# Kernel tuning notes

Measured on AMD Instinct MI355X. Metric: run time of the kernel, lower is better.

The kernel has to match this reference:

```python
import jax, jax.numpy as jnp
import numpy as np

B, N, C_IN = 2, 2048, 256
H, C_H = 8, 32  # no_heads, c_hidden; H*C_H == 256


def setup_inputs() -> dict:
    key = jax.random.key(0)
    ks = jax.random.split(key, 10)
    s_in = 1.0 / np.sqrt(C_IN)
    s_hid = 1.0 / np.sqrt(H * C_H)
    return {
        "q_x": jax.random.normal(ks[0], (B, N, C_IN), dtype=jnp.float32),
        "kv_x": jax.random.normal(ks[1], (B, N, C_IN), dtype=jnp.float32),
        "bias": jax.random.normal(ks[2], (B, H, N, N), dtype=jnp.float32),
        # Linear weights stored as [in, out] (transpose of torch layout)
        "Wq": jax.random.normal(ks[3], (C_IN, H * C_H), dtype=jnp.float32) * s_in,
        "Wk": jax.random.normal(ks[4], (C_IN, H * C_H), dtype=jnp.float32) * s_in,
        "Wv": jax.random.normal(ks[5], (C_IN, H * C_H), dtype=jnp.float32) * s_in,
        "Wg": jax.random.normal(ks[6], (C_IN, H * C_H), dtype=jnp.float32) * s_in,
        "bg": jnp.zeros((H * C_H,), dtype=jnp.float32),
        "Wo": jax.random.normal(ks[7], (H * C_H, C_IN), dtype=jnp.float32) * s_hid,
        "bo": jnp.zeros((C_IN,), dtype=jnp.float32),
    }


def reference(q_x, kv_x, bias, Wq, Wk, Wv, Wg, bg, Wo, bo):
    inv_sqrt = 1.0 / jnp.sqrt(jnp.asarray(C_H, q_x.dtype))
    # projections -> [B, N, H, C_H]
    q = (q_x @ Wq).reshape(B, N, H, C_H) * inv_sqrt
    k = (kv_x @ Wk).reshape(B, N, H, C_H)
    v = (kv_x @ Wv).reshape(B, N, H, C_H)
    # attention scores [B, H, Nq, Nk] with added pairwise bias
    a = jnp.einsum("bqhc,bkhc->bhqk", q, k) + bias
    a = jax.nn.softmax(a, axis=-1)
    o = jnp.einsum("bhqk,bkhc->bqhc", a, v)  # [B, N, H, C_H]
    # sigmoid gating
    g = jax.nn.sigmoid(q_x @ Wg + bg).reshape(B, N, H, C_H)
    o = o * g
    # output projection
    return o.reshape(B, N, H * C_H) @ Wo + bo
```

## Files before the change

kernel.cpp:

```cpp
#include <hip/hip_runtime.h>
#include <hip/hip_bf16.h>

#define B_   2
#define N_   2048
#define CIN  256
#define NH   8
#define CH   32

typedef unsigned short u16;
typedef __attribute__((ext_vector_type(4))) float f32x4;
typedef __bf16 bf16x8 __attribute__((ext_vector_type(8)));
typedef u16 u16x4 __attribute__((ext_vector_type(4)));
typedef u16 u16x8 __attribute__((ext_vector_type(8)));

static __device__ __forceinline__ u16 b16(float f) {
    __bf16 h = (__bf16)f;
    union { __bf16 h; u16 u; } c; c.h = h; return c.u;
}
static __device__ __forceinline__ float bf2f(u16 u) {
    union { unsigned u; float f; } c; c.u = ((unsigned)u) << 16; return c.f;
}
static __device__ __forceinline__ float sigmoidf_(float x) {
    return 1.0f / (1.0f + __expf(-x));
}
static __device__ __forceinline__ void gload_lds16(const void* g, void* lds) {
    __builtin_amdgcn_global_load_lds(
        (const __attribute__((address_space(1))) unsigned int*)g,
        (__attribute__((address_space(3))) unsigned int*)lds, 16, 0, 0);
}

__global__ __launch_bounds__(256)
void prep_kernel(const float* __restrict__ qx, const float* __restrict__ kvx,
                 u16* __restrict__ qxb, u16* __restrict__ kvxb,
                 const float* __restrict__ Wq, const float* __restrict__ Wk,
                 const float* __restrict__ Wv, const float* __restrict__ Wg,
                 const float* __restrict__ Wo,
                 u16* __restrict__ WqT, u16* __restrict__ WkT,
                 u16* __restrict__ WvT, u16* __restrict__ WgT,
                 u16* __restrict__ WoT)
{
    const int flat = blockIdx.x;
    const int tid = threadIdx.x;
    if (flat < 1024) {
        const int t = flat * 256 + tid;
        const int which = t >> 17;
        const size_t i = (size_t)(t & 131071) * 8;
        const float* s = which ? kvx : qx;
        u16* d = which ? kvxb : qxb;
        float4 a = *(const float4*)&s[i];
        float4 bv = *(const float4*)&s[i + 4];
        u16x8 o;
        o[0] = b16(a.x);  o[1] = b16(a.y);  o[2] = b16(a.z);  o[3] = b16(a.w);
        o[4] = b16(bv.x); o[5] = b16(bv.y); o[6] = b16(bv.z); o[7] = b16(bv.w);
        *(u16x8*)&d[i] = o;
        return;
    }
    const int wz = flat - 1024;
    const int z = wz >> 4, t16 = wz & 15;
    const int k0 = (t16 & 3) * 64, n0 = (t16 >> 2) * 64;
    const float* W = (z == 0) ? Wq : (z == 1) ? Wk : (z == 2) ? Wv : (z == 3) ? Wg : Wo;
    u16* Wt = (z == 0) ? WqT : (z == 1) ? WkT : (z == 2) ? WvT : (z == 3) ? WgT : WoT;
    const float s = (z == 0) ? 0.17677669529663687f : 1.0f;

    __shared__ float T[64][65];
    const int a = tid >> 4, c4 = (tid & 15) * 4;
#pragma unroll
    for (int i = 0; i < 4; i++) {
        float4 v = *(const float4*)&W[(size_t)(k0 + a + i * 16) * CIN + n0 + c4];
        T[a + i * 16][c4 + 0] = v.x * s; T[a + i * 16][c4 + 1] = v.y * s;
        T[a + i * 16][c4 + 2] = v.z * s; T[a + i * 16][c4 + 3] = v.w * s;
    }
    __syncthreads();
#pragma unroll
    for (int i = 0; i < 4; i++) {
        const int nr = a + i * 16;
        u16x4 o;
        o[0] = b16(T[c4 + 0][nr]); o[1] = b16(T[c4 + 1][nr]);
        o[2] = b16(T[c4 + 2][nr]); o[3] = b16(T[c4 + 3][nr]);
        *(u16x4*)&Wt[(size_t)(n0 + nr) * CIN + k0 + c4] = o;
    }
}

__global__ __launch_bounds__(256)
void proj_mfma(const u16* __restrict__ qxb, const u16* __restrict__ kvxb,
               const u16* __restrict__ WqT, const u16* __restrict__ WkT,
               const u16* __restrict__ WvT, const u16* __restrict__ WgT,
               const float* __restrict__ bgv,
               u16* __restrict__ Qw, u16* __restrict__ Kw,
               u16* __restrict__ Vt, u16* __restrict__ Gw)
{
    const int z = blockIdx.z;
    const int tid = threadIdx.x, w = tid >> 6, l = tid & 63, lr = l & 15, lq = l >> 4;
    f32x4 acc[4] = {{0,0,0,0},{0,0,0,0},{0,0,0,0},{0,0,0,0}};

    if (z != 2) {
        const u16* A = (z == 1) ? kvxb : qxb;
        const u16* W = (z == 0) ? WqT : (z == 1) ? WkT : WgT;
        const int m0 = blockIdx.y * 64 + w * 16;
        const int n0 = blockIdx.x * 64;
        const u16* Ap = A + (size_t)(m0 + lr) * CIN + lq * 8;
        const u16* Wp = W + (size_t)(n0 + lr) * CIN + lq * 8;
#pragma unroll
        for (int k0 = 0; k0 < CIN; k0 += 32) {
            bf16x8 af = *(const bf16x8*)(Ap + k0);
#pragma unroll
            for (int nt = 0; nt < 4; nt++) {
                bf16x8 bf = *(const bf16x8*)(Wp + (size_t)nt * 16 * CIN + k0);
                acc[nt] = __builtin_amdgcn_mfma_f32_16x16x32_bf16(af, bf, acc[nt], 0, 0, 0);
            }
        }
        if (z == 3) {
#pragma unroll
            for (int nt = 0; nt < 4; nt++) {
                const int col = n0 + nt * 16 + lr;
                const float bb = bgv[col];
#pragma unroll
                for (int r = 0; r < 4; r++)
                    Gw[(size_t)(m0 + lq * 4 + r) * CIN + col] = b16(sigmoidf_(acc[nt][r] + bb));
            }
        } else {
            u16* D = (z == 0) ? Qw : Kw;
#pragma unroll
            for (int nt = 0; nt < 4; nt++)
#pragma unroll
                for (int r = 0; r < 4; r++)
                    D[(size_t)(m0 + lq * 4 + r) * CIN + n0 + nt * 16 + lr] = b16(acc[nt][r]);
        }
    } else {
        const int c0 = blockIdx.x * 64 + w * 16;
        const int n0g = blockIdx.y * 64;
        const int bb_ = n0g >> 11, nl0 = n0g & (N_ - 1);
        const u16* Ap = WvT + (size_t)(c0 + lr) * CIN + lq * 8;
        const u16* Bp = kvxb + (size_t)(n0g + lr) * CIN + lq * 8;
#pragma unroll
        for (int k0 = 0; k0 < CIN; k0 += 32) {
            bf16x8 af = *(const bf16x8*)(Ap + k0);
#pragma unroll
            for (int nt = 0; nt < 4; nt++) {
                bf16x8 bf = *(const bf16x8*)(Bp + (size_t)nt * 16 * CIN + k0);
                acc[nt] = __builtin_amdgcn_mfma_f32_16x16x32_bf16(af, bf, acc[nt], 0, 0, 0);
            }
        }
#pragma unroll
        for (int nt = 0; nt < 4; nt++)
#pragma unroll
            for (int r = 0; r < 4; r++)
                Vt[((size_t)bb_ * CIN + c0 + lq * 4 + r) * N_ + nl0 + nt * 16 + lr] = b16(acc[nt][r]);
    }
}

#define RMAX(x) { x = fmaxf(x, __shfl_xor(x, 1)); x = fmaxf(x, __shfl_xor(x, 2)); \
                  x = fmaxf(x, __shfl_xor(x, 4)); x = fmaxf(x, __shfl_xor(x, 8)); }
#define RSUM(x) { x += __shfl_xor(x, 1); x += __shfl_xor(x, 2); \
                  x += __shfl_xor(x, 4); x += __shfl_xor(x, 8); }

__global__ __launch_bounds__(256)
void attn_kernel(const u16* __restrict__ Qw, const u16* __restrict__ Kw,
                 const u16* __restrict__ Vt, const float* __restrict__ bias,
                 const u16* __restrict__ Gw, u16* __restrict__ Owg)
{
    const int bid = blockIdx.x;
    const int h = bid & 7, qt = (bid >> 3) & 31, b = bid >> 8;
    const int tid = threadIdx.x;
    const int w = tid >> 6, l = tid & 63, lr = l & 15, lq = l >> 4;
    const int qb = qt * 64;

    __shared__ __align__(16) float Bt[4][3][16][32];
    __shared__ u16 Plds[4][8][4][16];

    const bf16x8 qf = *(const bf16x8*)(Qw + (size_t)(b * N_ + qb + w * 16 + lr) * CIN + h * CH + lq * 8);
    const u16* Kb = Kw + (size_t)(b * N_ + lr) * CIN + h * CH + lq * 8;
    const u16* Vb = Vt + (size_t)((b * NH + h) * CH + lr) * N_ + lq * 8;
    const float* biasW = bias + ((size_t)(b * NH + h) * N_ + qb + w * 16) * N_;

    const float* gl0 = biasW + (size_t)(l >> 3) * N_ + (l & 7) * 4;
    const float* gl1 = biasW + (size_t)(8 + (l >> 3)) * N_ + (l & 7) * 4;

#define STAGE(TT, BI) { \
    gload_lds16(gl0 + (size_t)(TT) * 32, &Bt[w][BI][0][0]); \
    gload_lds16(gl1 + (size_t)(TT) * 32, &Bt[w][BI][8][0]); }

#define KVLOAD(K) { kf0 = *(const bf16x8*)(Kb + (size_t)(K) * CIN); \
                    kf1 = *(const bf16x8*)(Kb + (size_t)((K) + 16) * CIN); \
                    vf0 = *(const bf16x8*)(Vb + (K)); \
                    vf1 = *(const bf16x8*)(Vb + 16 * N_ + (K)); }

    f32x4 acc0 = {0.f, 0.f, 0.f, 0.f}, acc1 = {0.f, 0.f, 0.f, 0.f};
    float m0v = 8.f, m1v = 8.f, m2v = 8.f, m3v = 8.f;
    float l0 = 0.f, l1 = 0.f, l2 = 0.f, l3 = 0.f;
    bf16x8 kf0, kf1, vf0, vf1;

    STAGE(0, 0)
    __builtin_amdgcn_sched_barrier(0);
    KVLOAD(0)
    __builtin_amdgcn_sched_barrier(0);
    STAGE(1, 1)
    __builtin_amdgcn_sched_barrier(0);

    int cur = 0, nxt = 2;
    for (int t = 0; t < 64; t++) {
        asm volatile("s_waitcnt vmcnt(2)" ::: "memory");
        const bf16x8 ck0 = kf0, ck1 = kf1, cv0 = vf0, cv1 = vf1;
        KVLOAD(((t + 1) & 63) * 32)
        __builtin_amdgcn_sched_barrier(0);
        STAGE((t + 2) & 63, nxt)
        __builtin_amdgcn_sched_barrier(0);

        const float* bt = &Bt[w][cur][lq * 4][0];
        f32x4 c0, c1;
        c0[0] = bt[0 * 32 + lr];      c0[1] = bt[1 * 32 + lr];
        c0[2] = bt[2 * 32 + lr];      c0[3] = bt[3 * 32 + lr];
        c1[0] = bt[0 * 32 + 16 + lr]; c1[1] = bt[1 * 32 + 16 + lr];
        c1[2] = bt[2 * 32 + 16 + lr]; c1[3] = bt[3 * 32 + 16 + lr];

        f32x4 s0 = __builtin_amdgcn_mfma_f32_16x16x32_bf16(qf, ck0, c0, 0, 0, 0);
        f32x4 s1 = __builtin_amdgcn_mfma_f32_16x16x32_bf16(qf, ck1, c1, 0, 0, 0);

        float pm0 = fmaxf(s0[0], s1[0]);
        float pm1 = fmaxf(s0[1], s1[1]);
        float pm2 = fmaxf(s0[2], s1[2]);
        float pm3 = fmaxf(s0[3], s1[3]);
        bool ev = (pm0 > m0v) || (pm1 > m1v) || (pm2 > m2v) || (pm3 > m3v);
        if (__any(ev)) {
            RMAX(pm0) RMAX(pm1) RMAX(pm2) RMAX(pm3)
            float t0 = fmaxf(m0v, pm0), t1 = fmaxf(m1v, pm1);
            float t2 = fmaxf(m2v, pm2), t3 = fmaxf(m3v, pm3);
            float sc0 = __expf(m0v - t0), sc1 = __expf(m1v - t1);
            float sc2 = __expf(m2v - t2), sc3 = __expf(m3v - t3);
            m0v = t0; m1v = t1; m2v = t2; m3v = t3;
            l0 *= sc0; l1 *= sc1; l2 *= sc2; l3 *= sc3;
            acc0[0] *= sc0; acc0[1] *= sc1; acc0[2] *= sc2; acc0[3] *= sc3;
            acc1[0] *= sc0; acc1[1] *= sc1; acc1[2] *= sc2; acc1[3] *= sc3;
        }
        float p00 = __expf(s0[0] - m0v), p01 = __expf(s0[1] - m1v);
        float p02 = __expf(s0[2] - m2v), p03 = __expf(s0[3] - m3v);
        float p10 = __expf(s1[0] - m0v), p11 = __expf(s1[1] - m1v);
        float p12 = __expf(s1[2] - m2v), p13 = __expf(s1[3] - m3v);
        l0 += p00 + p10; l1 += p01 + p11; l2 += p02 + p12; l3 += p03 + p13;

        u16* pw = &Plds[w][0][lq][lr];
        pw[0 * 64] = b16(p00); pw[1 * 64] = b16(p01);
        pw[2 * 64] = b16(p02); pw[3 * 64] = b16(p03);
        pw[4 * 64] = b16(p10); pw[5 * 64] = b16(p11);
        pw[6 * 64] = b16(p12); pw[7 * 64] = b16(p13);

        const bf16x8 pa = *(const bf16x8*)&Plds[w][(lq >> 1) * 4 + (lr & 3)][lr >> 2][(lq & 1) * 8];
        acc0 = __builtin_amdgcn_mfma_f32_16x16x32_bf16(pa, cv0, acc0, 0, 0, 0);
        acc1 = __builtin_amdgcn_mfma_f32_16x16x32_bf16(pa, cv1, acc1, 0, 0, 0);

        cur = (cur == 2) ? 0 : cur + 1;
        nxt = (nxt == 2) ? 0 : nxt + 1;
    }
#undef STAGE
#undef KVLOAD

    RSUM(l0) RSUM(l1) RSUM(l2) RSUM(l3)
    const float rr[4] = {1.0f / l0, 1.0f / l1, 1.0f / l2, 1.0f / l3};
    const f32x4 a0 = acc0, a1 = acc1;

    const u16* Gb = Gw + (size_t)(b * N_ + qb + w * 16 + lq * 4) * CIN + h * CH + lr;
    u16* Ob = Owg + (size_t)(b * N_ + qb + w * 16 + lq * 4) * CIN + h * CH + lr;
#pragma unroll
    for (int r = 0; r < 4; r++) {
        const float g0 = bf2f(Gb[r * CIN]), g1 = bf2f(Gb[r * CIN + 16]);
        Ob[r * CIN]      = b16(a0[r] * rr[r] * g0);
        Ob[r * CIN + 16] = b16(a1[r] * rr[r] * g1);
    }
}

__global__ __launch_bounds__(256)
void out_mfma(const u16* __restrict__ Owg, const u16* __restrict__ WoT,
              const float* __restrict__ bo, float* __restrict__ out)
{
    const int tid = threadIdx.x, w = tid >> 6, l = tid & 63, lr = l & 15, lq = l >> 4;
    const int m0 = blockIdx.y * 64 + w * 16, n0 = blockIdx.x * 64;
    const u16* Ap = Owg + (size_t)(m0 + lr) * CIN + lq * 8;
    const u16* Wp = WoT + (size_t)(n0 + lr) * CIN + lq * 8;
    f32x4 acc[4] = {{0,0,0,0},{0,0,0,0},{0,0,0,0},{0,0,0,0}};
#pragma unroll
    for (int k0 = 0; k0 < CIN; k0 += 32) {
        bf16x8 af = *(const bf16x8*)(Ap + k0);
#pragma unroll
        for (int nt = 0; nt < 4; nt++) {
            bf16x8 bf = *(const bf16x8*)(Wp + (size_t)nt * 16 * CIN + k0);
            acc[nt] = __builtin_amdgcn_mfma_f32_16x16x32_bf16(af, bf, acc[nt], 0, 0, 0);
        }
    }
#pragma unroll
    for (int nt = 0; nt < 4; nt++) {
        const float bb = bo[n0 + nt * 16 + lr];
#pragma unroll
        for (int r = 0; r < 4; r++)
            out[(size_t)(m0 + lq * 4 + r) * CIN + n0 + nt * 16 + lr] = acc[nt][r] + bb;
    }
}

extern "C" void kernel_launch(void* const* d_in, const int* in_sizes, int n_in,
                              void* d_out, int out_size, void* d_ws, size_t ws_size,
                              hipStream_t stream)
{
    const float* qx   = (const float*)d_in[0];
    const float* kvx  = (const float*)d_in[1];
    const float* bias = (const float*)d_in[2];
    const float* Wq = (const float*)d_in[3];
    const float* Wk = (const float*)d_in[4];
    const float* Wv = (const float*)d_in[5];
    const float* Wg = (const float*)d_in[6];
    const float* bg = (const float*)d_in[7];
    const float* Wo = (const float*)d_in[8];
    const float* bo = (const float*)d_in[9];
    float* out = (float*)d_out;

    char* ws = (char*)d_ws;
    const size_t SZB = (size_t)B_ * N_ * CIN * 2;
    u16* qxb  = (u16*)(ws + 0 * SZB);
    u16* kvxb = (u16*)(ws + 1 * SZB);
    u16* Qw   = (u16*)(ws + 2 * SZB);
    u16* Kw   = (u16*)(ws + 3 * SZB);
    u16* Vt   = (u16*)(ws + 4 * SZB);
    u16* Gw   = (u16*)(ws + 5 * SZB);
    u16* Owg  = (u16*)(ws + 6 * SZB);
    const size_t WSZ = (size_t)CIN * CIN * 2;
    u16* WqT = (u16*)(ws + 7 * SZB + 0 * WSZ);
    u16* WkT = (u16*)(ws + 7 * SZB + 1 * WSZ);
    u16* WvT = (u16*)(ws + 7 * SZB + 2 * WSZ);
    u16* WgT = (u16*)(ws + 7 * SZB + 3 * WSZ);
    u16* WoT = (u16*)(ws + 7 * SZB + 4 * WSZ);

    prep_kernel<<<dim3(1104), 256, 0, stream>>>(qx, kvx, qxb, kvxb,
                                                Wq, Wk, Wv, Wg, Wo,
                                                WqT, WkT, WvT, WgT, WoT);
    proj_mfma<<<dim3(4, 64, 4), 256, 0, stream>>>(qxb, kvxb, WqT, WkT, WvT, WgT,
                                                  bg, Qw, Kw, Vt, Gw);
    attn_kernel<<<dim3(512), 256, 0, stream>>>(Qw, Kw, Vt, bias, Gw, Owg);
    out_mfma<<<dim3(4, 64, 1), 256, 0, stream>>>(Owg, WoT, bo, out);
}
```

Before: 124.5 us.

## Stage projection and output GEMM operands through padded LDS with two-phase prefetch

The projection and output-projection GEMM kernels now load 64x128 tiles of both operands into padded shared memory with coalesced 16-byte loads, instead of each wave reading fragments straight from global memory. The second K half is prefetched into registers while the first half computes, giving a simple two-stage pipeline. Launch bounds now request four blocks per CU. The aim is to cut redundant, poorly coalesced global reads in the small GEMMs. The cost is about 34 KB of LDS per block plus extra barriers. The attention kernel is left alone, which holds most of the runtime.

```diff
diff --git a/kernel.cpp b/kernel.cpp
--- a/kernel.cpp
+++ b/kernel.cpp
@@ -81,7 +81,55 @@
     }
 }
 
-__global__ __launch_bounds__(256)
+#define LDW 136
+
+static __device__ __forceinline__ void stage_phase0(
+    const u16* __restrict__ src, u16 (*dst)[LDW], int tid)
+{
+#pragma unroll
+    for (int i = 0; i < 4; i++) {
+        const int e = tid + 256 * i;
+        const int row = e >> 4, c = e & 15;
+        bf16x8 v = *(const bf16x8*)(src + (size_t)row * CIN + c * 8);
+        *(bf16x8*)&dst[row][c * 8] = v;
+    }
+}
+static __device__ __forceinline__ void load_phase1(
+    const u16* __restrict__ src, bf16x8 r[4], int tid)
+{
+#pragma unroll
+    for (int i = 0; i < 4; i++) {
+        const int e = tid + 256 * i;
+        const int row = e >> 4, c = e & 15;
+        r[i] = *(const bf16x8*)(src + (size_t)row * CIN + 128 + c * 8);
+    }
+}
+static __device__ __forceinline__ void write_phase1(
+    const bf16x8 r[4], u16 (*dst)[LDW], int tid)
+{
+#pragma unroll
+    for (int i = 0; i < 4; i++) {
+        const int e = tid + 256 * i;
+        const int row = e >> 4, c = e & 15;
+        *(bf16x8*)&dst[row][c * 8] = r[i];
+    }
+}
+static __device__ __forceinline__ void compute_phase(
+    const u16 (*At)[LDW], const u16 (*Bt)[LDW],
+    int w, int lr, int lq, f32x4 acc[4])
+{
+#pragma unroll
+    for (int kk = 0; kk < 128; kk += 32) {
+        bf16x8 af = *(const bf16x8*)&At[w * 16 + lr][kk + lq * 8];
+#pragma unroll
+        for (int nt = 0; nt < 4; nt++) {
+            bf16x8 bf = *(const bf16x8*)&Bt[nt * 16 + lr][kk + lq * 8];
+            acc[nt] = __builtin_amdgcn_mfma_f32_16x16x32_bf16(af, bf, acc[nt], 0, 0, 0);
+        }
+    }
+}
+
+__global__ __launch_bounds__(256, 4)
 void proj_mfma(const u16* __restrict__ qxb, const u16* __restrict__ kvxb,
                const u16* __restrict__ WqT, const u16* __restrict__ WkT,
                const u16* __restrict__ WvT, const u16* __restrict__ WgT,
@@ -91,24 +139,38 @@
 {
     const int z = blockIdx.z;
     const int tid = threadIdx.x, w = tid >> 6, l = tid & 63, lr = l & 15, lq = l >> 4;
+
+    __shared__ u16 At[64][LDW];
+    __shared__ u16 Bt[64][LDW];
+
+    const u16* Arows;
+    const u16* Brows;
+    if (z != 2) {
+        Arows = ((z == 1) ? kvxb : qxb) + (size_t)(blockIdx.y * 64) * CIN;
+        Brows = ((z == 0) ? WqT : (z == 1) ? WkT : WgT) + (size_t)(blockIdx.x * 64) * CIN;
+    } else {
+        Arows = WvT + (size_t)(blockIdx.x * 64) * CIN;
+        Brows = kvxb + (size_t)(blockIdx.y * 64) * CIN;
+    }
+
     f32x4 acc[4] = {{0,0,0,0},{0,0,0,0},{0,0,0,0},{0,0,0,0}};
 
+    stage_phase0(Arows, At, tid);
+    stage_phase0(Brows, Bt, tid);
+    __syncthreads();
+    bf16x8 ra[4], rb[4];
+    load_phase1(Arows, ra, tid);
+    load_phase1(Brows, rb, tid);
+    compute_phase(At, Bt, w, lr, lq, acc);
+    __syncthreads();
+    write_phase1(ra, At, tid);
+    write_phase1(rb, Bt, tid);
+    __syncthreads();
+    compute_phase(At, Bt, w, lr, lq, acc);
+
     if (z != 2) {
-        const u16* A = (z == 1) ? kvxb : qxb;
-        const u16* W = (z == 0) ? WqT : (z == 1) ? WkT : WgT;
         const int m0 = blockIdx.y * 64 + w * 16;
         const int n0 = blockIdx.x * 64;
-        const u16* Ap = A + (size_t)(m0 + lr) * CIN + lq * 8;
-        const u16* Wp = W + (size_t)(n0 + lr) * CIN + lq * 8;
-#pragma unroll
-        for (int k0 = 0; k0 < CIN; k0 += 32) {
-            bf16x8 af = *(const bf16x8*)(Ap + k0);
-#pragma unroll
-            for (int nt = 0; nt < 4; nt++) {
-                bf16x8 bf = *(const bf16x8*)(Wp + (size_t)nt * 16 * CIN + k0);
-                acc[nt] = __builtin_amdgcn_mfma_f32_16x16x32_bf16(af, bf, acc[nt], 0, 0, 0);
-            }
-        }
         if (z == 3) {
 #pragma unroll
             for (int nt = 0; nt < 4; nt++) {
@@ -130,17 +192,6 @@
         const int c0 = blockIdx.x * 64 + w * 16;
         const int n0g = blockIdx.y * 64;
         const int bb_ = n0g >> 11, nl0 = n0g & (N_ - 1);
-        const u16* Ap = WvT + (size_t)(c0 + lr) * CIN + lq * 8;
-        const u16* Bp = kvxb + (size_t)(n0g + lr) * CIN + lq * 8;
-#pragma unroll
-        for (int k0 = 0; k0 < CIN; k0 += 32) {
-            bf16x8 af = *(const bf16x8*)(Ap + k0);
-#pragma unroll
-            for (int nt = 0; nt < 4; nt++) {
-                bf16x8 bf = *(const bf16x8*)(Bp + (size_t)nt * 16 * CIN + k0);
-                acc[nt] = __builtin_amdgcn_mfma_f32_16x16x32_bf16(af, bf, acc[nt], 0, 0, 0);
-            }
-        }
 #pragma unroll
         for (int nt = 0; nt < 4; nt++)
 #pragma unroll
@@ -165,7 +216,7 @@
     const int w = tid >> 6, l = tid & 63, lr = l & 15, lq = l >> 4;
     const int qb = qt * 64;
 
-    __shared__ __align__(16) float Bt[4][3][16][32];
+    __shared__ __align__(16) float Btl[4][3][16][32];
     __shared__ u16 Plds[4][8][4][16];
 
     const bf16x8 qf = *(const bf16x8*)(Qw + (size_t)(b * N_ + qb + w * 16 + lr) * CIN + h * CH + lq * 8);
@@ -177,8 +228,8 @@
     const float* gl1 = biasW + (size_t)(8 + (l >> 3)) * N_ + (l & 7) * 4;
 
 #define STAGE(TT, BI) { \
-    gload_lds16(gl0 + (size_t)(TT) * 32, &Bt[w][BI][0][0]); \
-    gload_lds16(gl1 + (size_t)(TT) * 32, &Bt[w][BI][8][0]); }
+    gload_lds16(gl0 + (size_t)(TT) * 32, &Btl[w][BI][0][0]); \
+    gload_lds16(gl1 + (size_t)(TT) * 32, &Btl[w][BI][8][0]); }
 
 #define KVLOAD(K) { kf0 = *(const bf16x8*)(Kb + (size_t)(K) * CIN); \
                     kf1 = *(const bf16x8*)(Kb + (size_t)((K) + 16) * CIN); \
@@ -206,7 +257,7 @@
         STAGE((t + 2) & 63, nxt)
         __builtin_amdgcn_sched_barrier(0);
 
-        const float* bt = &Bt[w][cur][lq * 4][0];
+        const float* bt = &Btl[w][cur][lq * 4][0];
         f32x4 c0, c1;
         c0[0] = bt[0 * 32 + lr];      c0[1] = bt[1 * 32 + lr];
         c0[2] = bt[2 * 32 + lr];      c0[3] = bt[3 * 32 + lr];
@@ -268,24 +319,34 @@
     }
 }
 
-__global__ __launch_bounds__(256)
+__global__ __launch_bounds__(256, 4)
 void out_mfma(const u16* __restrict__ Owg, const u16* __restrict__ WoT,
               const float* __restrict__ bo, float* __restrict__ out)
 {
     const int tid = threadIdx.x, w = tid >> 6, l = tid & 63, lr = l & 15, lq = l >> 4;
     const int m0 = blockIdx.y * 64 + w * 16, n0 = blockIdx.x * 64;
-    const u16* Ap = Owg + (size_t)(m0 + lr) * CIN + lq * 8;
-    const u16* Wp = WoT + (size_t)(n0 + lr) * CIN + lq * 8;
+
+    __shared__ u16 At[64][LDW];
+    __shared__ u16 Bt[64][LDW];
+
+    const u16* Arows = Owg + (size_t)(blockIdx.y * 64) * CIN;
+    const u16* Brows = WoT + (size_t)(blockIdx.x * 64) * CIN;
+
     f32x4 acc[4] = {{0,0,0,0},{0,0,0,0},{0,0,0,0},{0,0,0,0}};
-#pragma unroll
-    for (int k0 = 0; k0 < CIN; k0 += 32) {
-        bf16x8 af = *(const bf16x8*)(Ap + k0);
-#pragma unroll
-        for (int nt = 0; nt < 4; nt++) {
-            bf16x8 bf = *(const bf16x8*)(Wp + (size_t)nt * 16 * CIN + k0);
-            acc[nt] = __builtin_amdgcn_mfma_f32_16x16x32_bf16(af, bf, acc[nt], 0, 0, 0);
-        }
-    }
+
+    stage_phase0(Arows, At, tid);
+    stage_phase0(Brows, Bt, tid);
+    __syncthreads();
+    bf16x8 ra[4], rb[4];
+    load_phase1(Arows, ra, tid);
+    load_phase1(Brows, rb, tid);
+    compute_phase(At, Bt, w, lr, lq, acc);
+    __syncthreads();
+    write_phase1(ra, At, tid);
+    write_phase1(rb, Bt, tid);
+    __syncthreads();
+    compute_phase(At, Bt, w, lr, lq, acc);
+
 #pragma unroll
     for (int nt = 0; nt < 4; nt++) {
         const float bb = bo[n0 + nt * 16 + lr];
```

Measured after the change: 111.1 us. 1.12x faster.

## Fuse all stages into a persistent megakernel with atomic work queue and stage counters

Applied to the files above, without the earlier changes.

Replaces the four separate launches (prep, projections, attention, output projection) with one persistent kernel. Blocks pull work items from an atomic counter and wait on per-stage completion counters before consuming earlier results. The fp32 activation-to-bf16 conversion now happens inside the projection GEMM through LDS staging, so the separate qxb/kvxb round trip is gone. GEMMs now stage their tiles through LDS and prefetch the second K-half into registers. This is meant to remove launch gaps and tail effects between stages, at the cost of spin-waiting, a hipMemsetAsync per call, and coarse stage-level barriers that stop stages from overlapping much.

```diff
diff --git a/kernel.cpp b/kernel.cpp
--- a/kernel.cpp
+++ b/kernel.cpp
@@ -29,123 +29,60 @@
         (__attribute__((address_space(3))) unsigned int*)lds, 16, 0, 0);
 }
 
-__global__ __launch_bounds__(256)
-void prep_kernel(const float* __restrict__ qx, const float* __restrict__ kvx,
-                 u16* __restrict__ qxb, u16* __restrict__ kvxb,
-                 const float* __restrict__ Wq, const float* __restrict__ Wk,
-                 const float* __restrict__ Wv, const float* __restrict__ Wg,
-                 const float* __restrict__ Wo,
-                 u16* __restrict__ WqT, u16* __restrict__ WkT,
-                 u16* __restrict__ WvT, u16* __restrict__ WgT,
-                 u16* __restrict__ WoT)
+#define LDW 136
+
+typedef union {
+    float T[64][65];
+    struct { u16 At[64][LDW]; u16 Bt[64][LDW]; } g;
+    struct { float Btl[4][3][16][32]; u16 Plds[4][8][4][16]; } a;
+} SharedU;
+
+static __device__ __forceinline__ u16x8 cvt8(float4 a, float4 b) {
+    u16x8 o;
+    o[0] = b16(a.x); o[1] = b16(a.y); o[2] = b16(a.z); o[3] = b16(a.w);
+    o[4] = b16(b.x); o[5] = b16(b.y); o[6] = b16(b.z); o[7] = b16(b.w);
+    return o;
+}
+static __device__ __forceinline__ void stg_b16(const u16* __restrict__ src, u16 (*dst)[LDW], int tid) {
+#pragma unroll
+    for (int i = 0; i < 4; i++) {
+        const int e = tid + 256 * i, row = e >> 4, c = e & 15;
+        *(bf16x8*)&dst[row][c * 8] = *(const bf16x8*)(src + (size_t)row * CIN + c * 8);
+    }
+}
+static __device__ __forceinline__ void ld1_b16(const u16* __restrict__ src, bf16x8 r[4], int tid) {
+#pragma unroll
+    for (int i = 0; i < 4; i++) {
+        const int e = tid + 256 * i, row = e >> 4, c = e & 15;
+        r[i] = *(const bf16x8*)(src + (size_t)row * CIN + 128 + c * 8);
+    }
+}
+static __device__ __forceinline__ void wr1_b16(const bf16x8 r[4], u16 (*dst)[LDW], int tid) {
+#pragma unroll
+    for (int i = 0; i < 4; i++) {
+        const int e = tid + 256 * i, row = e >> 4, c = e & 15;
+        *(bf16x8*)&dst[row][c * 8] = r[i];
+    }
+}
+static __device__ __forceinline__ void stg_f32(const float* __restrict__ src, u16 (*dst)[LDW], int tid) {
+#pragma unroll
+    for (int i = 0; i < 4; i++) {
+        const int e = tid + 256 * i, row = e >> 4, c = e & 15;
+        const float* s = src + (size_t)row * CIN + c * 8;
+        *(u16x8*)&dst[row][c * 8] = cvt8(*(const float4*)s, *(const float4*)(s + 4));
+    }
+}
+static __device__ __forceinline__ void compute_phase(
+    const u16 (*At)[LDW], const u16 (*Bt)[LDW], int w, int lr, int lq, f32x4 acc[4])
 {
-    const int flat = blockIdx.x;
-    const int tid = threadIdx.x;
-    if (flat < 1024) {
-        const int t = flat * 256 + tid;
-        const int which = t >> 17;
-        const size_t i = (size_t)(t & 131071) * 8;
-        const float* s = which ? kvx : qx;
-        u16* d = which ? kvxb : qxb;
-        float4 a = *(const float4*)&s[i];
-        float4 bv = *(const float4*)&s[i + 4];
-        u16x8 o;
-        o[0] = b16(a.x);  o[1] = b16(a.y);  o[2] = b16(a.z);  o[3] = b16(a.w);
-        o[4] = b16(bv.x); o[5] = b16(bv.y); o[6] = b16(bv.z); o[7] = b16(bv.w);
-        *(u16x8*)&d[i] = o;
-        return;
-    }
-    const int wz = flat - 1024;
-    const int z = wz >> 4, t16 = wz & 15;
-    const int k0 = (t16 & 3) * 64, n0 = (t16 >> 2) * 64;
-    const float* W = (z == 0) ? Wq : (z == 1) ? Wk : (z == 2) ? Wv : (z == 3) ? Wg : Wo;
-    u16* Wt = (z == 0) ? WqT : (z == 1) ? WkT : (z == 2) ? WvT : (z == 3) ? WgT : WoT;
-    const float s = (z == 0) ? 0.17677669529663687f : 1.0f;
-
-    __shared__ float T[64][65];
-    const int a = tid >> 4, c4 = (tid & 15) * 4;
-#pragma unroll
-    for (int i = 0; i < 4; i++) {
-        float4 v = *(const float4*)&W[(size_t)(k0 + a + i * 16) * CIN + n0 + c4];
-        T[a + i * 16][c4 + 0] = v.x * s; T[a + i * 16][c4 + 1] = v.y * s;
-        T[a + i * 16][c4 + 2] = v.z * s; T[a + i * 16][c4 + 3] = v.w * s;
-    }
-    __syncthreads();
-#pragma unroll
-    for (int i = 0; i < 4; i++) {
-        const int nr = a + i * 16;
-        u16x4 o;
-        o[0] = b16(T[c4 + 0][nr]); o[1] = b16(T[c4 + 1][nr]);
-        o[2] = b16(T[c4 + 2][nr]); o[3] = b16(T[c4 + 3][nr]);
-        *(u16x4*)&Wt[(size_t)(n0 + nr) * CIN + k0 + c4] = o;
-    }
-}
-
-__global__ __launch_bounds__(256)
-void proj_mfma(const u16* __restrict__ qxb, const u16* __restrict__ kvxb,
-               const u16* __restrict__ WqT, const u16* __restrict__ WkT,
-               const u16* __restrict__ WvT, const u16* __restrict__ WgT,
-               const float* __restrict__ bgv,
-               u16* __restrict__ Qw, u16* __restrict__ Kw,
-               u16* __restrict__ Vt, u16* __restrict__ Gw)
-{
-    const int z = blockIdx.z;
-    const int tid = threadIdx.x, w = tid >> 6, l = tid & 63, lr = l & 15, lq = l >> 4;
-    f32x4 acc[4] = {{0,0,0,0},{0,0,0,0},{0,0,0,0},{0,0,0,0}};
-
-    if (z != 2) {
-        const u16* A = (z == 1) ? kvxb : qxb;
-        const u16* W = (z == 0) ? WqT : (z == 1) ? WkT : WgT;
-        const int m0 = blockIdx.y * 64 + w * 16;
-        const int n0 = blockIdx.x * 64;
-        const u16* Ap = A + (size_t)(m0 + lr) * CIN + lq * 8;
-        const u16* Wp = W + (size_t)(n0 + lr) * CIN + lq * 8;
-#pragma unroll
-        for (int k0 = 0; k0 < CIN; k0 += 32) {
-            bf16x8 af = *(const bf16x8*)(Ap + k0);
-#pragma unroll
-            for (int nt = 0; nt < 4; nt++) {
-                bf16x8 bf = *(const bf16x8*)(Wp + (size_t)nt * 16 * CIN + k0);
-                acc[nt] = __builtin_amdgcn_mfma_f32_16x16x32_bf16(af, bf, acc[nt], 0, 0, 0);
-            }
+#pragma unroll
+    for (int kk = 0; kk < 128; kk += 32) {
+        bf16x8 af = *(const bf16x8*)&At[w * 16 + lr][kk + lq * 8];
+#pragma unroll
+        for (int nt = 0; nt < 4; nt++) {
+            bf16x8 bf = *(const bf16x8*)&Bt[nt * 16 + lr][kk + lq * 8];
+            acc[nt] = __builtin_amdgcn_mfma_f32_16x16x32_bf16(af, bf, acc[nt], 0, 0, 0);
         }
-        if (z == 3) {
-#pragma unroll
-            for (int nt = 0; nt < 4; nt++) {
-                const int col = n0 + nt * 16 + lr;
-                const float bb = bgv[col];
-#pragma unroll
-                for (int r = 0; r < 4; r++)
-                    Gw[(size_t)(m0 + lq * 4 + r) * CIN + col] = b16(sigmoidf_(acc[nt][r] + bb));
-            }
-        } else {
-            u16* D = (z == 0) ? Qw : Kw;
-#pragma unroll
-            for (int nt = 0; nt < 4; nt++)
-#pragma unroll
-                for (int r = 0; r < 4; r++)
-                    D[(size_t)(m0 + lq * 4 + r) * CIN + n0 + nt * 16 + lr] = b16(acc[nt][r]);
-        }
-    } else {
-        const int c0 = blockIdx.x * 64 + w * 16;
-        const int n0g = blockIdx.y * 64;
-        const int bb_ = n0g >> 11, nl0 = n0g & (N_ - 1);
-        const u16* Ap = WvT + (size_t)(c0 + lr) * CIN + lq * 8;
-        const u16* Bp = kvxb + (size_t)(n0g + lr) * CIN + lq * 8;
-#pragma unroll
-        for (int k0 = 0; k0 < CIN; k0 += 32) {
-            bf16x8 af = *(const bf16x8*)(Ap + k0);
-#pragma unroll
-            for (int nt = 0; nt < 4; nt++) {
-                bf16x8 bf = *(const bf16x8*)(Bp + (size_t)nt * 16 * CIN + k0);
-                acc[nt] = __builtin_amdgcn_mfma_f32_16x16x32_bf16(af, bf, acc[nt], 0, 0, 0);
-            }
-        }
-#pragma unroll
-        for (int nt = 0; nt < 4; nt++)
-#pragma unroll
-            for (int r = 0; r < 4; r++)
-                Vt[((size_t)bb_ * CIN + c0 + lq * 4 + r) * N_ + nl0 + nt * 16 + lr] = b16(acc[nt][r]);
     }
 }
 
@@ -154,144 +91,292 @@
 #define RSUM(x) { x += __shfl_xor(x, 1); x += __shfl_xor(x, 2); \
                   x += __shfl_xor(x, 4); x += __shfl_xor(x, 8); }
 
+#define NIT0 80
+#define NIT1 1024
+#define NIT2 512
+#define NIT3 256
+#define IT1  (NIT0)
+#define IT2  (NIT0 + NIT1)
+#define IT3  (NIT0 + NIT1 + NIT2)
+#define ITOT (NIT0 + NIT1 + NIT2 + NIT3)
+
+static __device__ __forceinline__ void wait_done(unsigned* p, unsigned need) {
+    while (__hip_atomic_load(p, __ATOMIC_ACQUIRE, __HIP_MEMORY_SCOPE_AGENT) < need)
+        __builtin_amdgcn_s_sleep(8);
+}
+
 __global__ __launch_bounds__(256)
-void attn_kernel(const u16* __restrict__ Qw, const u16* __restrict__ Kw,
-                 const u16* __restrict__ Vt, const float* __restrict__ bias,
-                 const u16* __restrict__ Gw, u16* __restrict__ Owg)
+void mega_kernel(const float* __restrict__ qx, const float* __restrict__ kvx,
+                 const float* __restrict__ bias,
+                 const float* __restrict__ Wq, const float* __restrict__ Wk,
+                 const float* __restrict__ Wv, const float* __restrict__ Wg,
+                 const float* __restrict__ bgv,
+                 const float* __restrict__ Wo, const float* __restrict__ bo,
+                 u16* __restrict__ WqT, u16* __restrict__ WkT,
+                 u16* __restrict__ WvT, u16* __restrict__ WgT, u16* __restrict__ WoT,
+                 u16* __restrict__ Qw, u16* __restrict__ Kw,
+                 u16* __restrict__ Vt, u16* __restrict__ Gw, u16* __restrict__ Owg,
+                 float* __restrict__ out, unsigned* __restrict__ ctr)
 {
-    const int bid = blockIdx.x;
-    const int h = bid & 7, qt = (bid >> 3) & 31, b = bid >> 8;
     const int tid = threadIdx.x;
     const int w = tid >> 6, l = tid & 63, lr = l & 15, lq = l >> 4;
-    const int qb = qt * 64;
-
-    __shared__ __align__(16) float Bt[4][3][16][32];
-    __shared__ u16 Plds[4][8][4][16];
-
-    const bf16x8 qf = *(const bf16x8*)(Qw + (size_t)(b * N_ + qb + w * 16 + lr) * CIN + h * CH + lq * 8);
-    const u16* Kb = Kw + (size_t)(b * N_ + lr) * CIN + h * CH + lq * 8;
-    const u16* Vb = Vt + (size_t)((b * NH + h) * CH + lr) * N_ + lq * 8;
-    const float* biasW = bias + ((size_t)(b * NH + h) * N_ + qb + w * 16) * N_;
-
-    const float* gl0 = biasW + (size_t)(l >> 3) * N_ + (l & 7) * 4;
-    const float* gl1 = biasW + (size_t)(8 + (l >> 3)) * N_ + (l & 7) * 4;
+    __shared__ SharedU sh;
+    __shared__ int s_item;
+
+    for (;;) {
+        __syncthreads();
+        if (tid == 0) s_item = (int)atomicAdd(&ctr[0], 1u);
+        __syncthreads();
+        const int item = s_item;
+        if (item >= ITOT) return;
+
+        int stage;
+        if (item < IT1) {
+            stage = 0;
+            const int wz = item;
+            const int z = wz >> 4, t16 = wz & 15;
+            const int k0 = (t16 & 3) * 64, n0 = (t16 >> 2) * 64;
+            const float* W = (z == 0) ? Wq : (z == 1) ? Wk : (z == 2) ? Wv : (z == 3) ? Wg : Wo;
+            u16* Wt = (z == 0) ? WqT : (z == 1) ? WkT : (z == 2) ? WvT : (z == 3) ? WgT : WoT;
+            const float s = (z == 0) ? 0.17677669529663687f : 1.0f;
+            const int a = tid >> 4, c4 = (tid & 15) * 4;
+#pragma unroll
+            for (int i = 0; i < 4; i++) {
+                float4 v = *(const float4*)&W[(size_t)(k0 + a + i * 16) * CIN + n0 + c4];
+                sh.T[a + i * 16][c4 + 0] = v.x * s; sh.T[a + i * 16][c4 + 1] = v.y * s;
+                sh.T[a + i * 16][c4 + 2] = v.z * s; sh.T[a + i * 16][c4 + 3] = v.w * s;
+            }
+            __syncthreads();
+#pragma unroll
+            for (int i = 0; i < 4; i++) {
+                const int nr = a + i * 16;
+                u16x4 o;
+                o[0] = b16(sh.T[c4 + 0][nr]); o[1] = b16(sh.T[c4 + 1][nr]);
+                o[2] = b16(sh.T[c4 + 2][nr]); o[3] = b16(sh.T[c4 + 3][nr]);
+                *(u16x4*)&Wt[(size_t)(n0 + nr) * CIN + k0 + c4] = o;
+            }
+        } else if (item < IT2) {
+            stage = 1;
+            wait_done(&ctr[1], NIT0);
+            const int j = item - IT1;
+            const int z = j >> 8, y = (j >> 2) & 63, x = j & 3;
+            f32x4 acc[4] = {{0,0,0,0},{0,0,0,0},{0,0,0,0},{0,0,0,0}};
+
+            if (z != 2) {
+                const float* Af = ((z == 1) ? kvx : qx) + (size_t)(y * 64) * CIN;
+                const u16*   Bb = ((z == 0) ? WqT : (z == 1) ? WkT : WgT) + (size_t)(x * 64) * CIN;
+                stg_f32(Af, sh.g.At, tid);
+                stg_b16(Bb, sh.g.Bt, tid);
+                __syncthreads();
+                float4 raf[8]; bf16x8 rb[4];
+#pragma unroll
+                for (int i = 0; i < 4; i++) {
+                    const int e = tid + 256 * i, row = e >> 4, c = e & 15;
+                    const float* s = Af + (size_t)row * CIN + 128 + c * 8;
+                    raf[2 * i] = *(const float4*)s; raf[2 * i + 1] = *(const float4*)(s + 4);
+                }
+                ld1_b16(Bb, rb, tid);
+                compute_phase(sh.g.At, sh.g.Bt, w, lr, lq, acc);
+                __syncthreads();
+#pragma unroll
+                for (int i = 0; i < 4; i++) {
+                    const int e = tid + 256 * i, row = e >> 4, c = e & 15;
+                    *(u16x8*)&sh.g.At[row][c * 8] = cvt8(raf[2 * i], raf[2 * i + 1]);
+                }
+                wr1_b16(rb, sh.g.Bt, tid);
+                __syncthreads();
+                compute_phase(sh.g.At, sh.g.Bt, w, lr, lq, acc);
+
+                const int m0 = y * 64 + w * 16, n0 = x * 64;
+                if (z == 3) {
+#pragma unroll
+                    for (int nt = 0; nt < 4; nt++) {
+                        const int col = n0 + nt * 16 + lr;
+                        const float bb = bgv[col];
+#pragma unroll
+                        for (int r = 0; r < 4; r++)
+                            Gw[(size_t)(m0 + lq * 4 + r) * CIN + col] = b16(sigmoidf_(acc[nt][r] + bb));
+                    }
+                } else {
+                    u16* D = (z == 0) ? Qw : Kw;
+#pragma unroll
+                    for (int nt = 0; nt < 4; nt++)
+#pragma unroll
+                        for (int r = 0; r < 4; r++)
+                            D[(size_t)(m0 + lq * 4 + r) * CIN + n0 + nt * 16 + lr] = b16(acc[nt][r]);
+                }
+            } else {
+                const u16*   Ab = WvT + (size_t)(x * 64) * CIN;
+                const float* Bf = kvx + (size_t)(y * 64) * CIN;
+                stg_b16(Ab, sh.g.At, tid);
+                stg_f32(Bf, sh.g.Bt, tid);
+                __syncthreads();
+                bf16x8 ra[4]; float4 rbf[8];
+                ld1_b16(Ab, ra, tid);
+#pragma unroll
+                for (int i = 0; i < 4; i++) {
+                    const int e = tid + 256 * i, row = e >> 4, c = e & 15;
+                    const float* s = Bf + (size_t)row * CIN + 128 + c * 8;
+                    rbf[2 * i] = *(const float4*)s; rbf[2 * i + 1] = *(const float4*)(s + 4);
+                }
+                compute_phase(sh.g.At, sh.g.Bt, w, lr, lq, acc);
+                __syncthreads();
+                wr1_b16(ra, sh.g.At, tid);
+#pragma unroll
+                for (int i = 0; i < 4; i++) {
+                    const int e = tid + 256 * i, row = e >> 4, c = e & 15;
+                    *(u16x8*)&sh.g.Bt[row][c * 8] = cvt8(rbf[2 * i], rbf[2 * i + 1]);
+                }
+                __syncthreads();
+                compute_phase(sh.g.At, sh.g.Bt, w, lr, lq, acc);
+
+                const int c0 = x * 64 + w * 16;
+                const int n0g = y * 64;
+                const int bb_ = n0g >> 11, nl0 = n0g & (N_ - 1);
+#pragma unroll
+                for (int nt = 0; nt < 4; nt++)
+#pragma unroll
+                    for (int r = 0; r < 4; r++)
+                        Vt[((size_t)bb_ * CIN + c0 + lq * 4 + r) * N_ + nl0 + nt * 16 + lr] = b16(acc[nt][r]);
+            }
+        } else if (item < IT3) {
+            stage = 2;
+            wait_done(&ctr[2], NIT1);
+            const int bid = item - IT2;
+            const int h = bid & 7, qt = (bid >> 3) & 31, b = bid >> 8;
+            const int qb = qt * 64;
+
+            const bf16x8 qf = *(const bf16x8*)(Qw + (size_t)(b * N_ + qb + w * 16 + lr) * CIN + h * CH + lq * 8);
+            const u16* Kb = Kw + (size_t)(b * N_ + lr) * CIN + h * CH + lq * 8;
+            const u16* Vb = Vt + (size_t)((b * NH + h) * CH + lr) * N_ + lq * 8;
+            const float* biasW = bias + ((size_t)(b * NH + h) * N_ + qb + w * 16) * N_;
+            const float* gl0 = biasW + (size_t)(l >> 3) * N_ + (l & 7) * 4;
+            const float* gl1 = biasW + (size_t)(8 + (l >> 3)) * N_ + (l & 7) * 4;
 
 #define STAGE(TT, BI) { \
-    gload_lds16(gl0 + (size_t)(TT) * 32, &Bt[w][BI][0][0]); \
-    gload_lds16(gl1 + (size_t)(TT) * 32, &Bt[w][BI][8][0]); }
-
+    gload_lds16(gl0 + (size_t)(TT) * 32, &sh.a.Btl[w][BI][0][0]); \
+    gload_lds16(gl1 + (size_t)(TT) * 32, &sh.a.Btl[w][BI][8][0]); }
 #define KVLOAD(K) { kf0 = *(const bf16x8*)(Kb + (size_t)(K) * CIN); \
                     kf1 = *(const bf16x8*)(Kb + (size_t)((K) + 16) * CIN); \
                     vf0 = *(const bf16x8*)(Vb + (K)); \
                     vf1 = *(const bf16x8*)(Vb + 16 * N_ + (K)); }
 
-    f32x4 acc0 = {0.f, 0.f, 0.f, 0.f}, acc1 = {0.f, 0.f, 0.f, 0.f};
-    float m0v = 8.f, m1v = 8.f, m2v = 8.f, m3v = 8.f;
-    float l0 = 0.f, l1 = 0.f, l2 = 0.f, l3 = 0.f;
-    bf16x8 kf0, kf1, vf0, vf1;
-
-    STAGE(0, 0)
-    __builtin_amdgcn_sched_barrier(0);
-    KVLOAD(0)
-    __builtin_amdgcn_sched_barrier(0);
-    STAGE(1, 1)
-    __builtin_amdgcn_sched_barrier(0);
-
-    int cur = 0, nxt = 2;
-    for (int t = 0; t < 64; t++) {
-        asm volatile("s_waitcnt vmcnt(2)" ::: "memory");
-        const bf16x8 ck0 = kf0, ck1 = kf1, cv0 = vf0, cv1 = vf1;
-        KVLOAD(((t + 1) & 63) * 32)
-        __builtin_amdgcn_sched_barrier(0);
-        STAGE((t + 2) & 63, nxt)
-        __builtin_amdgcn_sched_barrier(0);
-
-        const float* bt = &Bt[w][cur][lq * 4][0];
-        f32x4 c0, c1;
-        c0[0] = bt[0 * 32 + lr];      c0[1] = bt[1 * 32 + lr];
-        c0[2] = bt[2 * 32 + lr];      c0[3] = bt[3 * 32 + lr];
-        c1[0] = bt[0 * 32 + 16 + lr]; c1[1] = bt[1 * 32 + 16 + lr];
-        c1[2] = bt[2 * 32 + 16 + lr]; c1[3] = bt[3 * 32 + 16 + lr];
-
-        f32x4 s0 = __builtin_amdgcn_mfma_f32_16x16x32_bf16(qf, ck0, c0, 0, 0, 0);
-        f32x4 s1 = __builtin_amdgcn_mfma_f32_16x16x32_bf16(qf, ck1, c1, 0, 0, 0);
-
-        float pm0 = fmaxf(s0[0], s1[0]);
-        float pm1 = fmaxf(s0[1], s1[1]);
-        float pm2 = fmaxf(s0[2], s1[2]);
-        float pm3 = fmaxf(s0[3], s1[3]);
-        bool ev = (pm0 > m0v) || (pm1 > m1v) || (pm2 > m2v) || (pm3 > m3v);
-        if (__any(ev)) {
-            RMAX(pm0) RMAX(pm1) RMAX(pm2) RMAX(pm3)
-            float t0 = fmaxf(m0v, pm0), t1 = fmaxf(m1v, pm1);
-            float t2 = fmaxf(m2v, pm2), t3 = fmaxf(m3v, pm3);
-            float sc0 = __expf(m0v - t0), sc1 = __expf(m1v - t1);
-            float sc2 = __expf(m2v - t2), sc3 = __expf(m3v - t3);
-            m0v = t0; m1v = t1; m2v = t2; m3v = t3;
-            l0 *= sc0; l1 *= sc1; l2 *= sc2; l3 *= sc3;
-            acc0[0] *= sc0; acc0[1] *= sc1; acc0[2] *= sc2; acc0[3] *= sc3;
-            acc1[0] *= sc0; acc1[1] *= sc1; acc1[2] *= sc2; acc1[3] *= sc3;
-        }
-        float p00 = __expf(s0[0] - m0v), p01 = __expf(s0[1] - m1v);
-        float p02 = __expf(s0[2] - m2v), p03 = __expf(s0[3] - m3v);
-        float p10 = __expf(s1[0] - m0v), p11 = __expf(s1[1] - m1v);
-        float p12 = __expf(s1[2] - m2v), p13 = __expf(s1[3] - m3v);
-        l0 += p00 + p10; l1 += p01 + p11; l2 += p02 + p12; l3 += p03 + p13;
-
-        u16* pw = &Plds[w][0][lq][lr];
-        pw[0 * 64] = b16(p00); pw[1 * 64] = b16(p01);
-        pw[2 * 64] = b16(p02); pw[3 * 64] = b16(p03);
-        pw[4 * 64] = b16(p10); pw[5 * 64] = b16(p11);
-        pw[6 * 64] = b16(p12); pw[7 * 64] = b16(p13);
-
-        const bf16x8 pa = *(const bf16x8*)&Plds[w][(lq >> 1) * 4 + (lr & 3)][lr >> 2][(lq & 1) * 8];
-        acc0 = __builtin_amdgcn_mfma_f32_16x16x32_bf16(pa, cv0, acc0, 0, 0, 0);
-        acc1 = __builtin_amdgcn_mfma_f32_16x16x32_bf16(pa, cv1, acc1, 0, 0, 0);
-
-        cur = (cur == 2) ? 0 : cur + 1;
-        nxt = (nxt == 2) ? 0 : nxt + 1;
-    }
+            f32x4 acc0 = {0.f, 0.f, 0.f, 0.f}, acc1 = {0.f, 0.f, 0.f, 0.f};
+            float m0v = 8.f, m1v = 8.f, m2v = 8.f, m3v = 8.f;
+            float l0 = 0.f, l1 = 0.f, l2 = 0.f, l3 = 0.f;
+            bf16x8 kf0, kf1, vf0, vf1;
+
+            STAGE(0, 0)
+            __builtin_amdgcn_sched_barrier(0);
+            KVLOAD(0)
+            __builtin_amdgcn_sched_barrier(0);
+            STAGE(1, 1)
+            __builtin_amdgcn_sched_barrier(0);
+
+            int cur = 0, nxt = 2;
+            for (int t = 0; t < 64; t++) {
+                asm volatile("s_waitcnt vmcnt(2)" ::: "memory");
+                const bf16x8 ck0 = kf0, ck1 = kf1, cv0 = vf0, cv1 = vf1;
+                KVLOAD(((t + 1) & 63) * 32)
+                __builtin_amdgcn_sched_barrier(0);
+                STAGE((t + 2) & 63, nxt)
+                __builtin_amdgcn_sched_barrier(0);
+
+                const float* bt = &sh.a.Btl[w][cur][lq * 4][0];
+                f32x4 c0, c1;
+                c0[0] = bt[0 * 32 + lr];      c0[1] = bt[1 * 32 + lr];
+                c0[2] = bt[2 * 32 + lr];      c0[3] = bt[3 * 32 + lr];
+                c1[0] = bt[0 * 32 + 16 + lr]; c1[1] = bt[1 * 32 + 16 + lr];
+                c1[2] = bt[2 * 32 + 16 + lr]; c1[3] = bt[3 * 32 + 16 + lr];
+
+                f32x4 s0 = __builtin_amdgcn_mfma_f32_16x16x32_bf16(qf, ck0, c0, 0, 0, 0);
+                f32x4 s1 = __builtin_amdgcn_mfma_f32_16x16x32_bf16(qf, ck1, c1, 0, 0, 0);
+
+                float pm0 = fmaxf(s0[0], s1[0]);
+                float pm1 = fmaxf(s0[1], s1[1]);
+                float pm2 = fmaxf(s0[2], s1[2]);
+                float pm3 = fmaxf(s0[3], s1[3]);
+                bool ev = (pm0 > m0v) || (pm1 > m1v) || (pm2 > m2v) || (pm3 > m3v);
+                if (__any(ev)) {
+                    RMAX(pm0) RMAX(pm1) RMAX(pm2) RMAX(pm3)
+                    float t0 = fmaxf(m0v, pm0), t1 = fmaxf(m1v, pm1);
+                    float t2 = fmaxf(m2v, pm2), t3 = fmaxf(m3v, pm3);
+                    float sc0 = __expf(m0v - t0), sc1 = __expf(m1v - t1);
+                    float sc2 = __expf(m2v - t2), sc3 = __expf(m3v - t3);
+                    m0v = t0; m1v = t1; m2v = t2; m3v = t3;
+                    l0 *= sc0; l1 *= sc1; l2 *= sc2; l3 *= sc3;
+                    acc0[0] *= sc0; acc0[1] *= sc1; acc0[2] *= sc2; acc0[3] *= sc3;
+                    acc1[0] *= sc0; acc1[1] *= sc1; acc1[2] *= sc2; acc1[3] *= sc3;
+                }
+                float p00 = __expf(s0[0] - m0v), p01 = __expf(s0[1] - m1v);
+                float p02 = __expf(s0[2] - m2v), p03 = __expf(s0[3] - m3v);
+                float p10 = __expf(s1[0] - m0v), p11 = __expf(s1[1] - m1v);
+                float p12 = __expf(s1[2] - m2v), p13 = __expf(s1[3] - m3v);
+                l0 += p00 + p10; l1 += p01 + p11; l2 += p02 + p12; l3 += p03 + p13;
+
+                u16* pw = &sh.a.Plds[w][0][lq][lr];
+                pw[0 * 64] = b16(p00); pw[1 * 64] = b16(p01);
+                pw[2 * 64] = b16(p02); pw[3 * 64] = b16(p03);
+                pw[4 * 64] = b16(p10); pw[5 * 64] = b16(p11);
+                pw[6 * 64] = b16(p12); pw[7 * 64] = b16(p13);
+
+                const bf16x8 pa = *(const bf16x8*)&sh.a.Plds[w][(lq >> 1) * 4 + (lr & 3)][lr >> 2][(lq & 1) * 8];
+                acc0 = __builtin_amdgcn_mfma_f32_16x16x32_bf16(pa, cv0, acc0, 0, 0, 0);
+                acc1 = __builtin_amdgcn_mfma_f32_16x16x32_bf16(pa, cv1, acc1, 0, 0, 0);
+
+                cur = (cur == 2) ? 0 : cur + 1;
+                nxt = (nxt == 2) ? 0 : nxt + 1;
+            }
 #undef STAGE
 #undef KVLOAD
 
-    RSUM(l0) RSUM(l1) RSUM(l2) RSUM(l3)
-    const float rr[4] = {1.0f / l0, 1.0f / l1, 1.0f / l2, 1.0f / l3};
-    const f32x4 a0 = acc0, a1 = acc1;
-
-    const u16* Gb = Gw + (size_t)(b * N_ + qb + w * 16 + lq * 4) * CIN + h * CH + lr;
-    u16* Ob = Owg + (size_t)(b * N_ + qb + w * 16 + lq * 4) * CIN + h * CH + lr;
-#pragma unroll
-    for (int r = 0; r < 4; r++) {
-        const float g0 = bf2f(Gb[r * CIN]), g1 = bf2f(Gb[r * CIN + 16]);
-        Ob[r * CIN]      = b16(a0[r] * rr[r] * g0);
-        Ob[r * CIN + 16] = b16(a1[r] * rr[r] * g1);
-    }
-}
-
-__global__ __launch_bounds__(256)
-void out_mfma(const u16* __restrict__ Owg, const u16* __restrict__ WoT,
-              const float* __restrict__ bo, float* __restrict__ out)
-{
-    const int tid = threadIdx.x, w = tid >> 6, l = tid & 63, lr = l & 15, lq = l >> 4;
-    const int m0 = blockIdx.y * 64 + w * 16, n0 = blockIdx.x * 64;
-    const u16* Ap = Owg + (size_t)(m0 + lr) * CIN + lq * 8;
-    const u16* Wp = WoT + (size_t)(n0 + lr) * CIN + lq * 8;
-    f32x4 acc[4] = {{0,0,0,0},{0,0,0,0},{0,0,0,0},{0,0,0,0}};
-#pragma unroll
-    for (int k0 = 0; k0 < CIN; k0 += 32) {
-        bf16x8 af = *(const bf16x8*)(Ap + k0);
-#pragma unroll
-        for (int nt = 0; nt < 4; nt++) {
-            bf16x8 bf = *(const bf16x8*)(Wp + (size_t)nt * 16 * CIN + k0);
-            acc[nt] = __builtin_amdgcn_mfma_f32_16x16x32_bf16(af, bf, acc[nt], 0, 0, 0);
+            RSUM(l0) RSUM(l1) RSUM(l2) RSUM(l3)
+            const float rr[4] = {1.0f / l0, 1.0f / l1, 1.0f / l2, 1.0f / l3};
+            const f32x4 a0 = acc0, a1 = acc1;
+
+            const u16* Gb = Gw + (size_t)(b * N_ + qb + w * 16 + lq * 4) * CIN + h * CH + lr;
+            u16* Ob = Owg + (size_t)(b * N_ + qb + w * 16 + lq * 4) * CIN + h * CH + lr;
+#pragma unroll
+            for (int r = 0; r < 4; r++) {
+                const float g0 = bf2f(Gb[r * CIN]), g1 = bf2f(Gb[r * CIN + 16]);
+                Ob[r * CIN]      = b16(a0[r] * rr[r] * g0);
+                Ob[r * CIN + 16] = b16(a1[r] * rr[r] * g1);
+            }
+        } else {
+            stage = 3;
+            wait_done(&ctr[3], NIT2);
+            const int o = item - IT3;
+            const int y = o >> 2, x = o & 3;
+            const int m0 = y * 64 + w * 16, n0 = x * 64;
+            const u16* Arows = Owg + (size_t)(y * 64) * CIN;
+            const u16* Brows = WoT + (size_t)(x * 64) * CIN;
+            f32x4 acc[4] = {{0,0,0,0},{0,0,0,0},{0,0,0,0},{0,0,0,0}};
+
+            stg_b16(Arows, sh.g.At, tid);
+            stg_b16(Brows, sh.g.Bt, tid);
+            __syncthreads();
+            bf16x8 ra[4], rb[4];
+            ld1_b16(Arows, ra, tid);
+            ld1_b16(Brows, rb, tid);
+            compute_phase(sh.g.At, sh.g.Bt, w, lr, lq, acc);
+            __syncthreads();
+            wr1_b16(ra, sh.g.At, tid);
+            wr1_b16(rb, sh.g.Bt, tid);
+            __syncthreads();
+            compute_phase(sh.g.At, sh.g.Bt, w, lr, lq, acc);
+
+#pragma unroll
+            for (int nt = 0; nt < 4; nt++) {
+                const float bb = bo[n0 + nt * 16 + lr];
+#pragma unroll
+                for (int r = 0; r < 4; r++)
+                    out[(size_t)(m0 + lq * 4 + r) * CIN + n0 + nt * 16 + lr] = acc[nt][r] + bb;
+            }
         }
-    }
-#pragma unroll
-    for (int nt = 0; nt < 4; nt++) {
-        const float bb = bo[n0 + nt * 16 + lr];
-#pragma unroll
-        for (int r = 0; r < 4; r++)
-            out[(size_t)(m0 + lq * 4 + r) * CIN + n0 + nt * 16 + lr] = acc[nt][r] + bb;
+
+        __syncthreads();
+        if (tid == 0 && stage < 3)
+            __hip_atomic_fetch_add(&ctr[1 + stage], 1u, __ATOMIC_RELEASE, __HIP_MEMORY_SCOPE_AGENT);
     }
 }
 
@@ -313,8 +398,6 @@
 
     char* ws = (char*)d_ws;
     const size_t SZB = (size_t)B_ * N_ * CIN * 2;
-    u16* qxb  = (u16*)(ws + 0 * SZB);
-    u16* kvxb = (u16*)(ws + 1 * SZB);
     u16* Qw   = (u16*)(ws + 2 * SZB);
     u16* Kw   = (u16*)(ws + 3 * SZB);
     u16* Vt   = (u16*)(ws + 4 * SZB);
@@ -326,12 +409,11 @@
     u16* WvT = (u16*)(ws + 7 * SZB + 2 * WSZ);
     u16* WgT = (u16*)(ws + 7 * SZB + 3 * WSZ);
     u16* WoT = (u16*)(ws + 7 * SZB + 4 * WSZ);
-
-    prep_kernel<<<dim3(1104), 256, 0, stream>>>(qx, kvx, qxb, kvxb,
-                                                Wq, Wk, Wv, Wg, Wo,
-                                                WqT, WkT, WvT, WgT, WoT);
-    proj_mfma<<<dim3(4, 64, 4), 256, 0, stream>>>(qxb, kvxb, WqT, WkT, WvT, WgT,
-                                                  bg, Qw, Kw, Vt, Gw);
-    attn_kernel<<<dim3(512), 256, 0, stream>>>(Qw, Kw, Vt, bias, Gw, Owg);
-    out_mfma<<<dim3(4, 64, 1), 256, 0, stream>>>(Owg, WoT, bo, out);
-}
+    unsigned* ctr = (unsigned*)(ws + 7 * SZB + 5 * WSZ);
+
+    hipMemsetAsync(ctr, 0, 64, stream);
+    mega_kernel<<<dim3(1024), 256, 0, stream>>>(qx, kvx, bias, Wq, Wk, Wv, Wg,
+                                                bg, Wo, bo,
+                                                WqT, WkT, WvT, WgT, WoT,
+                                                Qw, Kw, Vt, Gw, Owg, out, ctr);
+}
```

After: 413.9 us. 3.32x slower.
